# Performance work log

Measured on AMD Instinct MI355X. Metric: run time of the kernel, lower is better.

The kernel has to match this reference:

```python
import jax, jax.numpy as jnp
import numpy as np

D_MODEL = 1024
N_HEADS = 16
K_TOP = 64
D_HEAD = D_MODEL // N_HEADS


def setup_inputs() -> dict:
    key = jax.random.key(0)
    ks = jax.random.split(key, 9)
    B, L = 8, 4096
    bound = 1.0 / np.sqrt(D_MODEL)  # nn.Linear default init range
    lin = lambda k: jax.random.uniform(k, (D_MODEL, D_MODEL), jnp.float32, -bound, bound)
    vec = lambda k: jax.random.uniform(k, (D_MODEL,), jnp.float32, -bound, bound)
    return {
        "query": jax.random.normal(ks[0], (B, L, D_MODEL), jnp.float32),
        "Wq": lin(ks[1]), "bq": vec(ks[2]),
        "Wk": lin(ks[3]), "bk": vec(ks[4]),
        "Wv": lin(ks[5]), "bv": vec(ks[6]),
        "Wo": lin(ks[7]), "bo": vec(ks[8]),
    }


def reference(query, Wq, bq, Wk, bk, Wv, bv, Wo, bo):
    B, L_q, D = query.shape
    L_k = L_q  # self-attention: key = value = query
    F_q = L_q // 2 + 1
    F_k = L_k // 2 + 1
    k_top = min(K_TOP, F_q)

    def proj(x, W, b):
        # (B, L, D) -> (B, H, L, d_head)
        return (x @ W + b).reshape(B, -1, N_HEADS, D_HEAD).transpose(0, 2, 1, 3)

    q = proj(query, Wq, bq)
    k = proj(query, Wk, bk)
    v = proj(query, Wv, bv)

    q_freq = jnp.fft.rfft(q, axis=2)  # (B, H, F_q, d_head) complex64
    k_freq = jnp.fft.rfft(k, axis=2)
    v_freq = jnp.fft.rfft(v, axis=2)

    # top-k frequency bins by mean spectral magnitude of the query
    q_energy = jnp.abs(q_freq).mean(axis=-1)  # (B, H, F_q)
    _, idx = jax.lax.top_k(q_energy, k_top)   # (B, H, k)
    mapped_idx = jnp.clip(
        jnp.round(idx.astype(jnp.float32) * (F_k - 1) / (F_q - 1)).astype(jnp.int32),
        0, F_k - 1)

    gather = lambda x, i: jnp.take_along_axis(x, i[..., None], axis=2)
    q_top = gather(q_freq, idx)          # (B, H, k, d_head)
    k_top_freq = gather(k_freq, mapped_idx)
    v_top = gather(v_freq, mapped_idx)

    eps = 1e-8
    attn_score = (q_top.real * k_top_freq.real).sum(-1) / (D_HEAD ** 0.5 + eps)
    attn = jax.nn.softmax(attn_score, axis=-1)[..., None]  # (B, H, k, 1)

    # fill spectrum with mean of query spectrum, then scatter attended bins
    q_mean_freq = q_freq.mean(axis=2, keepdims=True)  # (B, H, 1, d_head) complex
    out_freq = jnp.broadcast_to(q_mean_freq, (B, N_HEADS, F_q, D_HEAD))
    src = (attn * v_top.real).astype(out_freq.dtype)  # real -> complex (imag=0)
    bi = jnp.arange(B)[:, None, None]
    hi = jnp.arange(N_HEADS)[None, :, None]
    out_freq = out_freq.at[bi, hi, idx].set(src)

    out_time = jnp.fft.irfft(out_freq, n=L_q, axis=2)  # (B, H, L, d_head)
    out = out_time.transpose(0, 2, 1, 3).reshape(B, L_q, D)
    return out @ Wo + bo
```

## Files before the change

### kernel.cpp

```cpp
#include <hip/hip_runtime.h>
#include <math.h>
#include <stdint.h>


typedef _Float16 f16;
typedef _Float16 f16x8 __attribute__((ext_vector_type(8)));
typedef float f32x4 __attribute__((ext_vector_type(4)));

#define PI_F 3.14159265358979323846f
#define PADJ(j) ((j) + ((j) >> 3))

__device__ __forceinline__ void gl_lds16(const void* g, void* l) {
  __builtin_amdgcn_global_load_lds((const __attribute__((address_space(1))) void*)g,
                                   (__attribute__((address_space(3))) void*)l, 16, 0, 0);
}

__device__ __forceinline__ float2 cadd(float2 a, float2 b) { return make_float2(a.x + b.x, a.y + b.y); }
__device__ __forceinline__ float2 csub(float2 a, float2 b) { return make_float2(a.x - b.x, a.y - b.y); }
__device__ __forceinline__ float2 cmul(float2 a, float2 b) {
  return make_float2(a.x * b.x - a.y * b.y, a.x * b.y + a.y * b.x);
}
__device__ __forceinline__ float2 cmni(float2 a) { return make_float2(a.y, -a.x); }

__device__ __forceinline__ void stg4(const char* g, size_t stride, int kb, char* lds,
                                     int tid, int w, int swz) {
#pragma unroll
  for (int it = 0; it < 4; ++it) {
    int row = it * 32 + (tid >> 3);
    gl_lds16(g + (size_t)row * stride + kb + swz, lds + it * 4096 + w * 1024);
  }
}

__global__ __launch_bounds__(256) void k_tw(float2* __restrict__ twtab, float2* __restrict__ utab) {
  int j = blockIdx.x * 256 + threadIdx.x;
  if (j < 2048) {
    float ang = (float)j * (-6.28318530717958647692f / 2048.0f);
    twtab[j] = make_float2(cosf(ang), sinf(ang));
  } else if (j < 4097) {
    int f = j - 2048;
    float ang = (float)f * (-6.28318530717958647692f / 4096.0f);
    utab[f] = make_float2(cosf(ang), sinf(ang));
  }
}

__global__ __launch_bounds__(256) void k_prep(const float* __restrict__ Wq, const float* __restrict__ Wo,
                                              f16* __restrict__ WqT, f16* __restrict__ WoT) {
  __shared__ float t[32][33];
  const float* src = blockIdx.z ? Wo : Wq;
  f16* dst = blockIdx.z ? WoT : WqT;
  int c0 = blockIdx.x * 32, r0 = blockIdx.y * 32;
  int tx = threadIdx.x, ty = threadIdx.y;
#pragma unroll
  for (int yy = 0; yy < 4; ++yy)
    t[ty + yy * 8][tx] = src[(size_t)(r0 + ty + yy * 8) * 1024 + c0 + tx];
  __syncthreads();
#pragma unroll
  for (int yy = 0; yy < 4; ++yy)
    dst[(size_t)(c0 + ty + yy * 8) * 1024 + r0 + tx] = (f16)t[tx][ty + yy * 8];
}

__global__ __launch_bounds__(256) void k_prep2(const float* __restrict__ Wk, const float* __restrict__ Wv,
                                               f16* __restrict__ WkT, f16* __restrict__ WvT) {
  __shared__ float t[32][33];
  const float* src = blockIdx.z ? Wv : Wk;
  f16* dst = blockIdx.z ? WvT : WkT;
  int c0 = blockIdx.x * 32, r0 = blockIdx.y * 32;
  int tx = threadIdx.x, ty = threadIdx.y;
#pragma unroll
  for (int yy = 0; yy < 4; ++yy)
    t[ty + yy * 8][tx] = src[(size_t)(r0 + ty + yy * 8) * 1024 + c0 + tx];
  __syncthreads();
#pragma unroll
  for (int yy = 0; yy < 4; ++yy)
    dst[(size_t)(c0 + ty + yy * 8) * 1024 + r0 + tx] = (f16)t[tx][ty + yy * 8];
}

__global__ __launch_bounds__(256) void k_t1(const float* __restrict__ X, float* __restrict__ Xt) {
  __shared__ float t[32][33];
  int b = blockIdx.z;
  int l0 = blockIdx.x * 32, d0 = blockIdx.y * 32;
  int tx = threadIdx.x, ty = threadIdx.y;
#pragma unroll
  for (int yy = 0; yy < 4; ++yy)
    t[ty + yy * 8][tx] = X[((size_t)b * 4096 + l0 + ty + yy * 8) * 1024 + d0 + tx];
  __syncthreads();
#pragma unroll
  for (int yy = 0; yy < 4; ++yy)
    Xt[((size_t)b * 1024 + d0 + ty + yy * 8) * 4096 + l0 + tx] = t[tx][ty + yy * 8];
}

__device__ __forceinline__ void r8_stage(const float2* __restrict__ cur, float2* __restrict__ nxt,
                                         const float2* __restrict__ tw, int tid, int lg) {
  int Ls = 1 << lg;
  int p = tid >> lg, q = tid & (Ls - 1);
  float2 x[8];
#pragma unroll
  for (int u = 0; u < 8; ++u) x[u] = cur[PADJ(tid + 256 * u)];
  float2 s0 = cadd(x[0], x[4]), d0v = csub(x[0], x[4]);
  float2 s1 = cadd(x[2], x[6]), d1v = csub(x[2], x[6]);
  float2 e0 = cadd(s0, s1), e2 = csub(s0, s1);
  float2 md1 = cmni(d1v);
  float2 e1 = cadd(d0v, md1), e3 = csub(d0v, md1);
  float2 t0 = cadd(x[1], x[5]), u0 = csub(x[1], x[5]);
  float2 t1 = cadd(x[3], x[7]), u1 = csub(x[3], x[7]);
  float2 o0 = cadd(t0, t1), o2 = csub(t0, t1);
  float2 mu1 = cmni(u1);
  float2 o1 = cadd(u0, mu1), o3 = csub(u0, mu1);
  const float C8 = 0.70710678118654752440f;
  float2 w1 = make_float2(C8 * (o1.x + o1.y), C8 * (o1.y - o1.x));
  float2 w2 = cmni(o2);
  float2 w3 = make_float2(C8 * (o3.y - o3.x), -C8 * (o3.x + o3.y));
  float2 y[8];
  y[0] = cadd(e0, o0); y[4] = csub(e0, o0);
  y[1] = cadd(e1, w1); y[5] = csub(e1, w1);
  y[2] = cadd(e2, w2); y[6] = csub(e2, w2);
  y[3] = cadd(e3, w3); y[7] = csub(e3, w3);
  int tb = p << lg;
#pragma unroll
  for (int v = 1; v < 8; ++v) y[v] = cmul(y[v], tw[tb * v]);
  int ob = q + (p << (lg + 3));
#pragma unroll
  for (int v = 0; v < 8; ++v) nxt[PADJ(ob + (v << lg))] = y[v];
}

__global__ __launch_bounds__(256) void k_fft(const float* __restrict__ Xt,
                                             const float2* __restrict__ twtab,
                                             const float2* __restrict__ utab,
                                             f16* __restrict__ PReU, f16* __restrict__ PImU,
                                             float* __restrict__ sumXf) {
  __shared__ float2 bufA[2304];
  __shared__ float2 bufB[2304];
  __shared__ float redr[256], redi[256];
  int tid = threadIdx.x;
  int blk = blockIdx.x;

  const float4* src = (const float4*)(Xt + (size_t)blk * 4096);
#pragma unroll
  for (int r = 0; r < 4; ++r) {
    int i4 = r * 256 + tid;
    float4 v = src[i4];
    bufA[PADJ(2 * i4)] = make_float2(v.x, v.y);
    bufA[PADJ(2 * i4 + 1)] = make_float2(v.z, v.w);
  }
  __syncthreads();
  r8_stage(bufA, bufB, twtab, tid, 0);
  __syncthreads();
  r8_stage(bufB, bufA, twtab, tid, 3);
  __syncthreads();
  r8_stage(bufA, bufB, twtab, tid, 6);
  __syncthreads();
#pragma unroll
  for (int h = 0; h < 2; ++h) {
    int i = (h << 8) + tid;
    float2 a0 = bufB[PADJ(i)], a1 = bufB[PADJ(i + 512)];
    float2 a2 = bufB[PADJ(i + 1024)], a3 = bufB[PADJ(i + 1536)];
    float2 s02 = cadd(a0, a2), d02 = csub(a0, a2);
    float2 s13 = cadd(a1, a3), d13m = cmni(csub(a1, a3));
    bufA[PADJ(i)] = cadd(s02, s13);
    bufA[PADJ(i + 512)] = cadd(d02, d13m);
    bufA[PADJ(i + 1024)] = csub(s02, s13);
    bufA[PADJ(i + 1536)] = csub(d02, d13m);
  }
  __syncthreads();
  float sumr = 0.f, sumi = 0.f;
  size_t obase = (size_t)blk * 2049;
  for (int f = tid; f <= 2048; f += 256) {
    int fz = f & 2047, fm = (2048 - f) & 2047;
    float2 z = bufA[PADJ(fz)], m = bufA[PADJ(fm)];
    float Er = 0.5f * (z.x + m.x), Ei = 0.5f * (z.y - m.y);
    float Or = 0.5f * (z.y + m.y), Oi = -0.5f * (z.x - m.x);
    float2 wv = utab[f];
    float Xr = Er + wv.x * Or - wv.y * Oi;
    float Xi = Ei + wv.x * Oi + wv.y * Or;
    PReU[obase + f] = (f16)Xr;
    PImU[obase + f] = (f16)Xi;
    sumr += Xr; sumi += Xi;
  }
  __syncthreads();
  redr[tid] = sumr; redi[tid] = sumi;
  __syncthreads();
  for (int s = 128; s > 0; s >>= 1) {
    if (tid < s) { redr[tid] += redr[tid + s]; redi[tid] += redi[tid + s]; }
    __syncthreads();
  }
  if (tid == 0) { sumXf[2 * blk] = redr[0]; sumXf[2 * blk + 1] = redi[0]; }
}

__global__ __launch_bounds__(256) void k_C(const float* __restrict__ sumXf, const float* __restrict__ Wq,
                                           const float* __restrict__ bq,
                                           float* __restrict__ Cre, float* __restrict__ Cim) {
  int b = blockIdx.x >> 2;
  int hd = ((blockIdx.x & 3) << 8) + threadIdx.x;
  float accr = 0.f, acci = 0.f;
  for (int dm = 0; dm < 1024; ++dm) {
    float w = Wq[(size_t)dm * 1024 + hd];
    accr += sumXf[2 * (b * 1024 + dm)] * w;
    acci += sumXf[2 * (b * 1024 + dm) + 1] * w;
  }
  Cre[b * 1024 + hd] = (accr + 4096.0f * bq[hd]) * (1.0f / 2049.0f);
  Cim[b * 1024 + hd] = acci * (1.0f / 2049.0f);
}

__global__ __launch_bounds__(256) void k_t2(const f16* __restrict__ PReU, const f16* __restrict__ PImU,
                                            f16* __restrict__ PT) {
  __shared__ f16 t[32][33];
  int z = blockIdx.z;
  int b = z >> 1, pl = z & 1;
  const f16* src = pl ? PImU : PReU;
  int f0 = blockIdx.x * 32, d0 = blockIdx.y * 32;
  int tx = threadIdx.x, ty = threadIdx.y;
#pragma unroll
  for (int yy = 0; yy < 4; ++yy) {
    int ff = f0 + tx;
    t[ty + yy * 8][tx] = (ff < 2049) ? src[(size_t)(b * 1024 + d0 + ty + yy * 8) * 2049 + ff] : (f16)0.f;
  }
  __syncthreads();
#pragma unroll
  for (int yy = 0; yy < 4; ++yy)
    PT[((size_t)b * 4352 + 2 * (f0 + ty + yy * 8) + pl) * 1024 + d0 + tx] = t[tx][ty + yy * 8];
}

__global__ __launch_bounds__(256, 2) void k_energy(const f16* __restrict__ PT, const f16* __restrict__ WqT,
                                                   const float* __restrict__ bq, float* __restrict__ energy) {
  __shared__ __align__(16) f16 sA[2][128 * 64];
  __shared__ __align__(16) f16 sB[2][128 * 64];
  int tid = threadIdx.x;
  int lane = tid & 63, w = tid >> 6;
  int lin = blockIdx.x;
  int xq = lin & 7, rq = lin >> 3;
  int bN = rq & 7;
  int Mblk = ((rq >> 3) << 3) + xq;
  int wr = w >> 1, wc = w & 1;
  f32x4 acc[4][4];
#pragma unroll
  for (int mf = 0; mf < 4; ++mf)
#pragma unroll
    for (int nf = 0; nf < 4; ++nf) acc[mf][nf] = 0;

  const char* gA0 = (const char*)PT + (size_t)(Mblk * 128) * 2048;
  const char* gB0 = (const char*)WqT + (size_t)(bN * 128) * 2048;
  int swz = ((tid & 7) ^ ((tid >> 3) & 7)) << 4;
  int r = lane & 15, q = lane >> 4;
  int cq = q << 4;

  stg4(gA0, 2048, 0, (char*)&sA[0][0], tid, w, swz);
  stg4(gB0, 2048, 0, (char*)&sB[0][0], tid, w, swz);
  for (int ks = 0; ks < 16; ++ks) {
    int cur = ks & 1;
    if (ks < 15) {
      int kb = (ks + 1) * 128;
      stg4(gA0, 2048, kb, (char*)&sA[cur ^ 1][0], tid, w, swz);
      stg4(gB0, 2048, kb, (char*)&sB[cur ^ 1][0], tid, w, swz);
      asm volatile("s_waitcnt vmcnt(8)\ns_barrier" ::: "memory");
    } else {
      asm volatile("s_waitcnt vmcnt(0)\ns_barrier" ::: "memory");
    }
    const char* bA = (const char*)&sA[cur][0];
    const char* bB = (const char*)&sB[cur][0];
#pragma unroll
    for (int kk = 0; kk < 64; kk += 32) {
      int cb = (kk << 1) + cq;
      f16x8 aF[4], bF[4];
#pragma unroll
      for (int mf = 0; mf < 4; ++mf) {
        int row = wr * 64 + mf * 16 + r;
        aF[mf] = *(const f16x8*)(bA + row * 128 + (cb ^ ((row & 7) << 4)));
      }
#pragma unroll
      for (int nf = 0; nf < 4; ++nf) {
        int row = wc * 64 + nf * 16 + r;
        bF[nf] = *(const f16x8*)(bB + row * 128 + (cb ^ ((row & 7) << 4)));
      }
#pragma unroll
      for (int mf = 0; mf < 4; ++mf)
#pragma unroll
        for (int nf = 0; nf < 4; ++nf)
          acc[mf][nf] = __builtin_amdgcn_mfma_f32_16x16x32_f16(aF[mf], bF[nf], acc[mf][nf], 0, 0, 0);
    }
    asm volatile("s_barrier" ::: "memory");
  }
  int b = Mblk / 34;
  int tIb = Mblk - b * 34;
  int head = 2 * bN + wc;
  bool dc = (tIb == 0 && wr == 0 && q == 0);
#pragma unroll
  for (int mf = 0; mf < 4; ++mf) {
    float sE = 0.f, sO = 0.f;
#pragma unroll
    for (int nf = 0; nf < 4; ++nf) {
      float re0 = acc[mf][nf][0], im0 = acc[mf][nf][1];
      float re1 = acc[mf][nf][2], im1 = acc[mf][nf][3];
      if (dc && mf == 0) re0 += 4096.0f * bq[head * 64 + nf * 16 + r];
      sE += sqrtf(re0 * re0 + im0 * im0);
      sO += sqrtf(re1 * re1 + im1 * im1);
    }
#pragma unroll
    for (int off = 1; off < 16; off <<= 1) {
      sE += __shfl_xor(sE, off);
      sO += __shfl_xor(sO, off);
    }
    if (r == 0) {
      int fp = tIb * 64 + wr * 32 + mf * 8 + (q << 1);
      energy[((size_t)b * 16 + head) * 2176 + fp] = sE * 0.015625f;
      energy[((size_t)b * 16 + head) * 2176 + fp + 1] = sO * 0.015625f;
    }
  }
}

__global__ __launch_bounds__(256) void k_topk(const float* __restrict__ energy, int* __restrict__ idxb) {
  __shared__ float vals[2049];
  __shared__ unsigned long long wbest[4];
  int tid = threadIdx.x, bh = blockIdx.x;
  const float* e = energy + (size_t)bh * 2176;
  for (int i = tid; i < 2049; i += 256) vals[i] = e[i];
  __syncthreads();
  for (int it = 0; it < 64; ++it) {
    unsigned long long best = 0ull;
    for (int f = tid; f < 2049; f += 256) {
      unsigned b32 = __float_as_uint(vals[f]);
      b32 = (b32 & 0x80000000u) ? ~b32 : (b32 | 0x80000000u);
      unsigned long long k = ((unsigned long long)b32 << 12) | (unsigned)(4095 - f);
      best = (k > best) ? k : best;
    }
#pragma unroll
    for (int off = 32; off > 0; off >>= 1) {
      unsigned long long o = __shfl_xor(best, off);
      best = (o > best) ? o : best;
    }
    if ((tid & 63) == 0) wbest[tid >> 6] = best;
    __syncthreads();
    if (tid == 0) {
      unsigned long long b0 = wbest[0] > wbest[1] ? wbest[0] : wbest[1];
      unsigned long long b1 = wbest[2] > wbest[3] ? wbest[2] : wbest[3];
      unsigned long long bb = b0 > b1 ? b0 : b1;
      int f = 4095 - (int)(bb & 4095ull);
      idxb[bh * 64 + it] = f;
      vals[f] = -1.0f;
    }
    __syncthreads();
  }
}

__global__ __launch_bounds__(256) void k_qkv(const f16* __restrict__ PT, const int* __restrict__ idxb,
                                             const f16* __restrict__ WqT, const f16* __restrict__ WkT,
                                             const f16* __restrict__ WvT, float* __restrict__ part) {
  __shared__ __align__(16) f16 sA[64 * 64];
  __shared__ __align__(16) f16 sB[192 * 64];
  __shared__ int fjs[64];
  int tid = threadIdx.x, lane = tid & 63, w = tid >> 6;
  int bh = blockIdx.x, ks = blockIdx.y;
  int b = bh >> 4, h = bh & 15;
  if (tid < 64) fjs[tid] = idxb[bh * 64 + tid];
  __syncthreads();
  f32x4 acc[4][3];
#pragma unroll
  for (int mf = 0; mf < 4; ++mf)
#pragma unroll
    for (int nf = 0; nf < 3; ++nf) acc[mf][nf] = 0;

  int l8 = lane & 7;
  int lr = lane >> 3;
  int swz = (l8 ^ lr) << 4;

  for (int kt = 0; kt < 4; ++kt) {
    int kbyte = ks * 512 + kt * 128;
#pragma unroll
    for (int t = 0; t < 2; ++t) {
      int ia = w * 2 + t;
      int row = ia * 8 + lr;
      const char* src = (const char*)PT + (size_t)(b * 4352 + 2 * fjs[row]) * 2048 + kbyte + swz;
      gl_lds16(src, (char*)sA + ia * 1024);
    }
#pragma unroll
    for (int t = 0; t < 6; ++t) {
      int ib = w * 6 + t;
      int row = ib * 8 + lr;
      const f16* Wt = (row < 64) ? WqT : (row < 128) ? WkT : WvT;
      const char* src = (const char*)Wt + (size_t)(h * 64 + (row & 63)) * 2048 + kbyte + swz;
      gl_lds16(src, (char*)sB + ib * 1024);
    }
    __syncthreads();
#pragma unroll
    for (int kk = 0; kk < 64; kk += 32) {
      int cb = (kk << 1) + ((lane >> 4) << 4);
      int r = lane & 15;
      f16x8 aF[4], bF[3];
#pragma unroll
      for (int mf = 0; mf < 4; ++mf) {
        int row = mf * 16 + r;
        aF[mf] = *(const f16x8*)((const char*)sA + row * 128 + (cb ^ ((row & 7) << 4)));
      }
#pragma unroll
      for (int nf = 0; nf < 3; ++nf) {
        int row = w * 48 + nf * 16 + r;
        bF[nf] = *(const f16x8*)((const char*)sB + row * 128 + (cb ^ ((row & 7) << 4)));
      }
#pragma unroll
      for (int mf = 0; mf < 4; ++mf)
#pragma unroll
        for (int nf = 0; nf < 3; ++nf)
          acc[mf][nf] = __builtin_amdgcn_mfma_f32_16x16x32_f16(aF[mf], bF[nf], acc[mf][nf], 0, 0, 0);
    }
    __syncthreads();
  }
  float* pb = part + (size_t)(ks * 128 + bh) * 12288;
#pragma unroll
  for (int mf = 0; mf < 4; ++mf)
#pragma unroll
    for (int nf = 0; nf < 3; ++nf)
#pragma unroll
      for (int rr = 0; rr < 4; ++rr) {
        int m = mf * 16 + ((lane >> 4) << 2) + rr;
        int n = w * 48 + nf * 16 + (lane & 15);
        pb[m * 192 + n] = acc[mf][nf][rr];
      }
}

__global__ __launch_bounds__(256) void k_attn2(const float* __restrict__ part, const int* __restrict__ idxb,
                                               const float* __restrict__ bq, const float* __restrict__ bk,
                                               const float* __restrict__ bv, const float* __restrict__ Cre,
                                               float* __restrict__ amp) {
  __shared__ float sQKV[64][196];
  __shared__ float scores[64], attns[64];
  __shared__ int fjs[64];
  __shared__ int dcrow;
  int tid = threadIdx.x, bh = blockIdx.x;
  int b = bh >> 4, h = bh & 15;
  if (tid == 0) dcrow = -1;
  __syncthreads();
  if (tid < 64) {
    int f = idxb[bh * 64 + tid];
    fjs[tid] = f;
    if (f == 0) dcrow = tid;
  }
  __syncthreads();
  const float4* p0 = (const float4*)(part + (size_t)bh * 12288);
  const size_t s4 = (size_t)128 * 12288 / 4;
#pragma unroll
  for (int it = 0; it < 12; ++it) {
    int e = it * 256 + tid;
    float4 v0 = p0[e], v1 = p0[e + s4], v2 = p0[e + 2 * s4], v3 = p0[e + 3 * s4];
    float4 v;
    v.x = v0.x + v1.x + v2.x + v3.x;
    v.y = v0.y + v1.y + v2.y + v3.y;
    v.z = v0.z + v1.z + v2.z + v3.z;
    v.w = v0.w + v1.w + v2.w + v3.w;
    int m = e / 48, n0 = (e % 48) * 4;
    *(float4*)&sQKV[m][n0] = v;
  }
  __syncthreads();
  if (dcrow >= 0 && tid < 192) {
    const float* bias = (tid < 64) ? bq : (tid < 128) ? bk : bv;
    sQKV[dcrow][tid] += 4096.0f * bias[h * 64 + (tid & 63)];
  }
  __syncthreads();
  {
    int j = tid >> 2, p = tid & 3;
    float s = 0.f;
#pragma unroll
    for (int c = 0; c < 16; ++c) {
      int cc = p * 16 + c;
      s = fmaf(sQKV[j][cc], sQKV[j][64 + cc], s);
    }
    s += __shfl_xor(s, 1);
    s += __shfl_xor(s, 2);
    if (p == 0) scores[j] = s * 0.125f;
  }
  __syncthreads();
  if (tid < 64) {
    float s = scores[tid];
    float m = s;
#pragma unroll
    for (int off = 32; off > 0; off >>= 1) m = fmaxf(m, __shfl_xor(m, off));
    float ev = expf(s - m);
    float sm = ev;
#pragma unroll
    for (int off = 32; off > 0; off >>= 1) sm += __shfl_xor(sm, off);
    attns[tid] = ev / sm;
  }
  __syncthreads();
  {
    int j = tid >> 2, d0 = (tid & 3) * 16;
    float at = attns[j];
    int fj = fjs[j];
    float wj = (fj == 0 || fj == 2048) ? 0.5f : 1.0f;
    float* ao = amp + ((size_t)bh * 64 + j) * 64 + d0;
#pragma unroll
    for (int q4 = 0; q4 < 4; ++q4) {
      float4 c4 = *(const float4*)&Cre[b * 1024 + h * 64 + d0 + q4 * 4];
      float4 vv = *(const float4*)&sQKV[j][128 + d0 + q4 * 4];
      float4 av;
      av.x = wj * (at * vv.x - c4.x);
      av.y = wj * (at * vv.y - c4.y);
      av.z = wj * (at * vv.z - c4.z);
      av.w = wj * (at * vv.w - c4.w);
      *(float4*)&ao[q4 * 4] = av;
    }
  }
}

__global__ __launch_bounds__(256) void k_ot(const float* __restrict__ amp, const int* __restrict__ idxb,
                                            const float* __restrict__ Cre, const float* __restrict__ Cim,
                                            f16* __restrict__ OT) {
  __shared__ __align__(16) float sAmp[64][64];
  __shared__ __align__(16) float sCre[64];
  __shared__ __align__(16) float sCim[64];
  __shared__ int fjs[64];
  int tid = threadIdx.x;
  int bh = blockIdx.x >> 4, tch = blockIdx.x & 15;
  int b = bh >> 4, h = bh & 15;
  for (int e = tid; e < 4096; e += 256) ((float*)sAmp)[e] = amp[(size_t)bh * 4096 + e];
  if (tid < 64) {
    sCre[tid] = Cre[b * 1024 + h * 64 + tid];
    sCim[tid] = Cim[b * 1024 + h * 64 + tid];
    fjs[tid] = idxb[bh * 64 + tid];
  }
  __syncthreads();
  int t = tch * 256 + tid;
  float4 acc[16];
#pragma unroll
  for (int d4 = 0; d4 < 16; ++d4) acc[d4] = make_float4(0.f, 0.f, 0.f, 0.f);
  float ssum = 0.f;
  for (int jj = 0; jj < 64; ++jj) {
    int r = (fjs[jj] * t) & 4095;
    float ang = (float)r * 0.00153398078788564123f;
    float sn, cs;
    __sincosf(ang, &sn, &cs);
    ssum += sn;
    const float4* arow = (const float4*)&sAmp[jj][0];
#pragma unroll
    for (int d4 = 0; d4 < 16; ++d4) {
      float4 a = arow[d4];
      acc[d4].x = fmaf(a.x, cs, acc[d4].x);
      acc[d4].y = fmaf(a.y, cs, acc[d4].y);
      acc[d4].z = fmaf(a.z, cs, acc[d4].z);
      acc[d4].w = fmaf(a.w, cs, acc[d4].w);
    }
  }
  float g = ssum;
  if (t & 1) {
    int tp = (t <= 2048) ? t : 4096 - t;
    float sg = (t <= 2048) ? 1.f : -1.f;
    float aa = (float)tp * (PI_F / 4096.0f);
    g -= sg * (cosf(aa) / sinf(aa));
  }
  const float s2L = 2.0f / 4096.0f;
  int isT0 = (t == 0);
  f16* o16 = OT + ((size_t)bh * 4096 + t) * 64;
#pragma unroll
  for (int d4 = 0; d4 < 16; ++d4) {
    float4 ci4 = *(const float4*)&sCim[d4 * 4];
    float4 cr4 = *(const float4*)&sCre[d4 * 4];
    acc[d4].x = s2L * (acc[d4].x + ci4.x * g) + (isT0 ? cr4.x : 0.f);
    acc[d4].y = s2L * (acc[d4].y + ci4.y * g) + (isT0 ? cr4.y : 0.f);
    acc[d4].z = s2L * (acc[d4].z + ci4.z * g) + (isT0 ? cr4.z : 0.f);
    acc[d4].w = s2L * (acc[d4].w + ci4.w * g) + (isT0 ? cr4.w : 0.f);
  }
#pragma unroll
  for (int p = 0; p < 8; ++p) {
    float4 a = acc[2 * p], bb = acc[2 * p + 1];
    f16x8 v;
    v[0] = (f16)a.x; v[1] = (f16)a.y; v[2] = (f16)a.z; v[3] = (f16)a.w;
    v[4] = (f16)bb.x; v[5] = (f16)bb.y; v[6] = (f16)bb.z; v[7] = (f16)bb.w;
    *(f16x8*)(o16 + p * 8) = v;
  }
}

__global__ __launch_bounds__(256, 2) void k_final(const f16* __restrict__ OT, const f16* __restrict__ WoT,
                                                  const float* __restrict__ bo, float* __restrict__ out) {
  __shared__ __align__(16) f16 sA[2][128 * 64];
  __shared__ __align__(16) f16 sB[2][128 * 64];
  int tid = threadIdx.x, lane = tid & 63, wv = tid >> 6;
  int lin = blockIdx.x;
  int xq = lin & 7, rq = lin >> 3;
  int bN = rq & 7;
  int Mblk = ((rq >> 3) << 3) + xq;
  int wr = wv >> 1, wc = wv & 1;
  f32x4 acc[4][4];
#pragma unroll
  for (int mf = 0; mf < 4; ++mf)
#pragma unroll
    for (int nf = 0; nf < 4; ++nf) acc[mf][nf] = 0;
  int b = Mblk >> 5, t0 = (Mblk & 31) * 128;
  const char* gB0 = (const char*)WoT + (size_t)(bN * 128) * 2048;
  int swz = ((tid & 7) ^ ((tid >> 3) & 7)) << 4;
  int r = lane & 15, q = lane >> 4;
  int cq = q << 4;
#define GA_TILE(ks) ((const char*)OT + (size_t)((b * 16 + (ks)) * 4096 + t0) * 128)

  stg4(GA_TILE(0), 128, 0, (char*)&sA[0][0], tid, wv, swz);
  stg4(gB0, 2048, 0, (char*)&sB[0][0], tid, wv, swz);
  for (int ks = 0; ks < 16; ++ks) {
    int cur = ks & 1;
    if (ks < 15) {
      stg4(GA_TILE(ks + 1), 128, 0, (char*)&sA[cur ^ 1][0], tid, wv, swz);
      stg4(gB0, 2048, (ks + 1) * 128, (char*)&sB[cur ^ 1][0], tid, wv, swz);
      asm volatile("s_waitcnt vmcnt(8)\ns_barrier" ::: "memory");
    } else {
      asm volatile("s_waitcnt vmcnt(0)\ns_barrier" ::: "memory");
    }
    const char* bA = (const char*)&sA[cur][0];
    const char* bB = (const char*)&sB[cur][0];
#pragma unroll
    for (int kk = 0; kk < 64; kk += 32) {
      int cb = (kk << 1) + cq;
      f16x8 aF[4], bF[4];
#pragma unroll
      for (int mf = 0; mf < 4; ++mf) {
        int row = wr * 64 + mf * 16 + r;
        aF[mf] = *(const f16x8*)(bA + row * 128 + (cb ^ ((row & 7) << 4)));
      }
#pragma unroll
      for (int nf = 0; nf < 4; ++nf) {
        int row = wc * 64 + nf * 16 + r;
        bF[nf] = *(const f16x8*)(bB + row * 128 + (cb ^ ((row & 7) << 4)));
      }
#pragma unroll
      for (int mf = 0; mf < 4; ++mf)
#pragma unroll
        for (int nf = 0; nf < 4; ++nf)
          acc[mf][nf] = __builtin_amdgcn_mfma_f32_16x16x32_f16(aF[mf], bF[nf], acc[mf][nf], 0, 0, 0);
    }
    asm volatile("s_barrier" ::: "memory");
  }
#undef GA_TILE
#pragma unroll
  for (int nf = 0; nf < 4; ++nf) {
    int gcol = bN * 128 + wc * 64 + nf * 16 + r;
    float bcol = bo[gcol];
#pragma unroll
    for (int mf = 0; mf < 4; ++mf) {
#pragma unroll
      for (int rr = 0; rr < 4; ++rr) {
        int grow = Mblk * 128 + wr * 64 + mf * 16 + (q << 2) + rr;
        out[(size_t)grow * 1024 + gcol] = acc[mf][nf][rr] + bcol;
      }
    }
  }
}

extern "C" void kernel_launch(void* const* d_in, const int* in_sizes, int n_in,
                              void* d_out, int out_size, void* d_ws, size_t ws_size,
                              hipStream_t stream) {
  const float* X = (const float*)d_in[0];
  const float* Wq = (const float*)d_in[1];
  const float* bq = (const float*)d_in[2];
  const float* Wk = (const float*)d_in[3];
  const float* bk = (const float*)d_in[4];
  const float* Wv = (const float*)d_in[5];
  const float* bv = (const float*)d_in[6];
  const float* Wo = (const float*)d_in[7];
  const float* bo = (const float*)d_in[8];
  float* out = (float*)d_out;

  if (ws_size < 208928768ULL) return;
  char* w = (char*)d_ws;
  float* Xt = (float*)(w);
  f16* PT = (f16*)(w);
  f16* WkT = (f16*)(w + 71303168);
  f16* WvT = (f16*)(w + 73400320);
  float* part = (float*)(w + 75497472);
  char* R2 = w + 134217728;
  f16* PReU = (f16*)(R2);
  f16* PImU = (f16*)(R2 + 33570816);
  f16* OT = (f16*)(R2);
  char* R3 = R2 + 67141632;
  float* sumXf = (float*)(R3);
  float* Cre = (float*)(R3 + 65536);
  float* Cim = (float*)(R3 + 98304);
  float* energy = (float*)(R3 + 131072);
  int* idxb = (int*)(R3 + 1245184);
  float* amp = (float*)(R3 + 1277952);
  f16* WqT = (f16*)(R3 + 3375104);
  f16* WoT = (f16*)(R3 + 5472256);
  float2* twtab = (float2*)d_out;
  float2* utab = twtab + 2048;

  dim3 b32(32, 8);
  hipLaunchKernelGGL(k_tw, dim3(17), dim3(256), 0, stream, twtab, utab);
  hipLaunchKernelGGL(k_prep, dim3(32, 32, 2), b32, 0, stream, Wq, Wo, WqT, WoT);
  hipLaunchKernelGGL(k_t1, dim3(128, 32, 8), b32, 0, stream, X, Xt);
  hipLaunchKernelGGL(k_fft, dim3(8192), dim3(256), 0, stream, Xt, twtab, utab, PReU, PImU, sumXf);
  hipLaunchKernelGGL(k_prep2, dim3(32, 32, 2), b32, 0, stream, Wk, Wv, WkT, WvT);
  hipLaunchKernelGGL(k_C, dim3(32), dim3(256), 0, stream, sumXf, Wq, bq, Cre, Cim);
  hipLaunchKernelGGL(k_t2, dim3(68, 32, 16), b32, 0, stream, PReU, PImU, PT);
  hipLaunchKernelGGL(k_energy, dim3(2176), dim3(256), 0, stream, PT, WqT, bq, energy);
  hipLaunchKernelGGL(k_topk, dim3(128), dim3(256), 0, stream, energy, idxb);
  hipLaunchKernelGGL(k_qkv, dim3(128, 4), dim3(256), 0, stream, PT, idxb, WqT, WkT, WvT, part);
  hipLaunchKernelGGL(k_attn2, dim3(128), dim3(256), 0, stream, part, idxb, bq, bk, bv, Cre, amp);
  hipLaunchKernelGGL(k_ot, dim3(2048), dim3(256), 0, stream, amp, idxb, Cre, Cim, OT);
  hipLaunchKernelGGL(k_final, dim3(2048), dim3(256), 0, stream, OT, WoT, bo, out);
}
```

Baseline: 573.7 us.

## Compute sparse inverse DFT in k_ot with f16 MFMA instead of scalar FMAs

After: 526.8 us. -8.2%, faster.

```diff
diff --git a/kernel.cpp b/kernel.cpp
--- a/kernel.cpp
+++ b/kernel.cpp
@@ -419,7 +419,7 @@
 __global__ __launch_bounds__(256) void k_attn2(const float* __restrict__ part, const int* __restrict__ idxb,
                                                const float* __restrict__ bq, const float* __restrict__ bk,
                                                const float* __restrict__ bv, const float* __restrict__ Cre,
-                                               float* __restrict__ amp) {
+                                               f16* __restrict__ ampT) {
   __shared__ float sQKV[64][196];
   __shared__ float scores[64], attns[64];
   __shared__ int fjs[64];
@@ -484,85 +484,119 @@
     float at = attns[j];
     int fj = fjs[j];
     float wj = (fj == 0 || fj == 2048) ? 0.5f : 1.0f;
-    float* ao = amp + ((size_t)bh * 64 + j) * 64 + d0;
 #pragma unroll
     for (int q4 = 0; q4 < 4; ++q4) {
       float4 c4 = *(const float4*)&Cre[b * 1024 + h * 64 + d0 + q4 * 4];
       float4 vv = *(const float4*)&sQKV[j][128 + d0 + q4 * 4];
-      float4 av;
-      av.x = wj * (at * vv.x - c4.x);
-      av.y = wj * (at * vv.y - c4.y);
-      av.z = wj * (at * vv.z - c4.z);
-      av.w = wj * (at * vv.w - c4.w);
-      *(float4*)&ao[q4 * 4] = av;
-    }
-  }
-}
-
-__global__ __launch_bounds__(256) void k_ot(const float* __restrict__ amp, const int* __restrict__ idxb,
+      float av0 = wj * (at * vv.x - c4.x);
+      float av1 = wj * (at * vv.y - c4.y);
+      float av2 = wj * (at * vv.z - c4.z);
+      float av3 = wj * (at * vv.w - c4.w);
+      f16* o = ampT + (size_t)bh * 4096 + (d0 + q4 * 4) * 64 + j;
+      o[0] = (f16)av0; o[64] = (f16)av1; o[128] = (f16)av2; o[192] = (f16)av3;
+    }
+  }
+}
+
+__global__ __launch_bounds__(256) void k_ot(const f16* __restrict__ ampT, const int* __restrict__ idxb,
                                             const float* __restrict__ Cre, const float* __restrict__ Cim,
                                             f16* __restrict__ OT) {
-  __shared__ __align__(16) float sAmp[64][64];
-  __shared__ __align__(16) float sCre[64];
-  __shared__ __align__(16) float sCim[64];
+  __shared__ __align__(16) f16 sAmp[64][72];
+  __shared__ float gbuf[256];
   __shared__ int fjs[64];
-  int tid = threadIdx.x;
+  int tid = threadIdx.x, lane = tid & 63, w = tid >> 6;
   int bh = blockIdx.x >> 4, tch = blockIdx.x & 15;
   int b = bh >> 4, h = bh & 15;
-  for (int e = tid; e < 4096; e += 256) ((float*)sAmp)[e] = amp[(size_t)bh * 4096 + e];
-  if (tid < 64) {
-    sCre[tid] = Cre[b * 1024 + h * 64 + tid];
-    sCim[tid] = Cim[b * 1024 + h * 64 + tid];
-    fjs[tid] = idxb[bh * 64 + tid];
-  }
-  __syncthreads();
-  int t = tch * 256 + tid;
-  float4 acc[16];
-#pragma unroll
-  for (int d4 = 0; d4 < 16; ++d4) acc[d4] = make_float4(0.f, 0.f, 0.f, 0.f);
-  float ssum = 0.f;
-  for (int jj = 0; jj < 64; ++jj) {
-    int r = (fjs[jj] * t) & 4095;
-    float ang = (float)r * 0.00153398078788564123f;
-    float sn, cs;
-    __sincosf(ang, &sn, &cs);
-    ssum += sn;
-    const float4* arow = (const float4*)&sAmp[jj][0];
-#pragma unroll
-    for (int d4 = 0; d4 < 16; ++d4) {
-      float4 a = arow[d4];
-      acc[d4].x = fmaf(a.x, cs, acc[d4].x);
-      acc[d4].y = fmaf(a.y, cs, acc[d4].y);
-      acc[d4].z = fmaf(a.z, cs, acc[d4].z);
-      acc[d4].w = fmaf(a.w, cs, acc[d4].w);
-    }
-  }
-  float g = ssum;
-  if (t & 1) {
-    int tp = (t <= 2048) ? t : 4096 - t;
-    float sg = (t <= 2048) ? 1.f : -1.f;
-    float aa = (float)tp * (PI_F / 4096.0f);
-    g -= sg * (cosf(aa) / sinf(aa));
-  }
+  if (tid < 64) fjs[tid] = idxb[bh * 64 + tid];
+  {
+    int row = tid >> 2, seg = tid & 3;
+    const f16* src = ampT + (size_t)bh * 4096 + row * 64 + seg * 16;
+    f16x8 v0 = *(const f16x8*)src;
+    f16x8 v1 = *(const f16x8*)(src + 8);
+    *(f16x8*)&sAmp[row][seg * 16] = v0;
+    *(f16x8*)&sAmp[row][seg * 16 + 8] = v1;
+  }
+  __syncthreads();
+  int r = lane & 15, q = lane >> 4;
+  int tbase = tch * 256 + w * 64;
+  const float cang = 0.00153398078788564123f;
+  f16x8 aF[4][2];
+  float ss[4];
+#pragma unroll
+  for (int mf = 0; mf < 4; ++mf) {
+    int t = tbase + mf * 16 + r;
+    float s = 0.f;
+#pragma unroll
+    for (int kk2 = 0; kk2 < 2; ++kk2) {
+      f16x8 a;
+#pragma unroll
+      for (int jj = 0; jj < 8; ++jj) {
+        int j = kk2 * 32 + q * 8 + jj;
+        int ridx = (fjs[j] * t) & 4095;
+        float sn, cs;
+        __sincosf((float)ridx * cang, &sn, &cs);
+        s += sn;
+        a[jj] = (f16)cs;
+      }
+      aF[mf][kk2] = a;
+    }
+    ss[mf] = s;
+  }
+#pragma unroll
+  for (int mf = 0; mf < 4; ++mf) {
+    ss[mf] += __shfl_xor(ss[mf], 16);
+    ss[mf] += __shfl_xor(ss[mf], 32);
+  }
+  if (q == 0) {
+#pragma unroll
+    for (int mf = 0; mf < 4; ++mf) {
+      int t = tbase + mf * 16 + r;
+      float g = ss[mf];
+      if (t & 1) {
+        int tp = (t <= 2048) ? t : 4096 - t;
+        float sg = (t <= 2048) ? 1.f : -1.f;
+        float aa = (float)tp * (PI_F / 4096.0f);
+        g -= sg * (cosf(aa) / sinf(aa));
+      }
+      gbuf[w * 64 + mf * 16 + r] = g;
+    }
+  }
+  f16x8 bF[4][2];
+#pragma unroll
+  for (int nf = 0; nf < 4; ++nf)
+#pragma unroll
+    for (int kk2 = 0; kk2 < 2; ++kk2)
+      bF[nf][kk2] = *(const f16x8*)&sAmp[nf * 16 + r][kk2 * 32 + q * 8];
+  f32x4 acc[4][4];
+#pragma unroll
+  for (int mf = 0; mf < 4; ++mf)
+#pragma unroll
+    for (int nf = 0; nf < 4; ++nf) acc[mf][nf] = 0;
+#pragma unroll
+  for (int kk2 = 0; kk2 < 2; ++kk2)
+#pragma unroll
+    for (int mf = 0; mf < 4; ++mf)
+#pragma unroll
+      for (int nf = 0; nf < 4; ++nf)
+        acc[mf][nf] = __builtin_amdgcn_mfma_f32_16x16x32_f16(aF[mf][kk2], bF[nf][kk2], acc[mf][nf], 0, 0, 0);
+  __syncthreads();
   const float s2L = 2.0f / 4096.0f;
-  int isT0 = (t == 0);
-  f16* o16 = OT + ((size_t)bh * 4096 + t) * 64;
-#pragma unroll
-  for (int d4 = 0; d4 < 16; ++d4) {
-    float4 ci4 = *(const float4*)&sCim[d4 * 4];
-    float4 cr4 = *(const float4*)&sCre[d4 * 4];
-    acc[d4].x = s2L * (acc[d4].x + ci4.x * g) + (isT0 ? cr4.x : 0.f);
-    acc[d4].y = s2L * (acc[d4].y + ci4.y * g) + (isT0 ? cr4.y : 0.f);
-    acc[d4].z = s2L * (acc[d4].z + ci4.z * g) + (isT0 ? cr4.z : 0.f);
-    acc[d4].w = s2L * (acc[d4].w + ci4.w * g) + (isT0 ? cr4.w : 0.f);
-  }
-#pragma unroll
-  for (int p = 0; p < 8; ++p) {
-    float4 a = acc[2 * p], bb = acc[2 * p + 1];
-    f16x8 v;
-    v[0] = (f16)a.x; v[1] = (f16)a.y; v[2] = (f16)a.z; v[3] = (f16)a.w;
-    v[4] = (f16)bb.x; v[5] = (f16)bb.y; v[6] = (f16)bb.z; v[7] = (f16)bb.w;
-    *(f16x8*)(o16 + p * 8) = v;
+#pragma unroll
+  for (int nf = 0; nf < 4; ++nf) {
+    int d = nf * 16 + r;
+    float cim = Cim[b * 1024 + h * 64 + d];
+    float cre = Cre[b * 1024 + h * 64 + d];
+#pragma unroll
+    for (int mf = 0; mf < 4; ++mf) {
+#pragma unroll
+      for (int rr = 0; rr < 4; ++rr) {
+        int ro = mf * 16 + q * 4 + rr;
+        int t = tbase + ro;
+        float g = gbuf[w * 64 + ro];
+        float val = s2L * (acc[mf][nf][rr] + cim * g) + ((t == 0) ? cre : 0.f);
+        OT[((size_t)bh * 4096 + t) * 64 + d] = (f16)val;
+      }
+    }
   }
 }
 
@@ -670,7 +704,7 @@
   float* Cim = (float*)(R3 + 98304);
   float* energy = (float*)(R3 + 131072);
   int* idxb = (int*)(R3 + 1245184);
-  float* amp = (float*)(R3 + 1277952);
+  f16* ampT = (f16*)(R3 + 1277952);
   f16* WqT = (f16*)(R3 + 3375104);
   f16* WoT = (f16*)(R3 + 5472256);
   float2* twtab = (float2*)d_out;
@@ -687,7 +721,7 @@
   hipLaunchKernelGGL(k_energy, dim3(2176), dim3(256), 0, stream, PT, WqT, bq, energy);
   hipLaunchKernelGGL(k_topk, dim3(128), dim3(256), 0, stream, energy, idxb);
   hipLaunchKernelGGL(k_qkv, dim3(128, 4), dim3(256), 0, stream, PT, idxb, WqT, WkT, WvT, part);
-  hipLaunchKernelGGL(k_attn2, dim3(128), dim3(256), 0, stream, part, idxb, bq, bk, bv, Cre, amp);
-  hipLaunchKernelGGL(k_ot, dim3(2048), dim3(256), 0, stream, amp, idxb, Cre, Cim, OT);
+  hipLaunchKernelGGL(k_attn2, dim3(128), dim3(256), 0, stream, part, idxb, bq, bk, bv, Cre, ampT);
+  hipLaunchKernelGGL(k_ot, dim3(2048), dim3(256), 0, stream, ampT, idxb, Cre, Cim, OT);
   hipLaunchKernelGGL(k_final, dim3(2048), dim3(256), 0, stream, OT, WoT, bo, out);
 }
```
